# Kernel tuning notes

Hardware: AMD Instinct MI355X
Metric: run time of the kernel (lower is better)

## Reference

```python
import jax, jax.numpy as jnp
import numpy as np

N_FEAT = 128      # node_feat_size
HID = 128         # hidden_size
NUM_SEM = 64
N_ITER = 2
E_TYPES = 8
MAX_CHILDS = 65536
NUM_EDGES = 1048576


def setup_inputs() -> dict:
    key = jax.random.key(0)
    ks = jax.random.split(key, 12)
    d_in = N_FEAT + NUM_SEM
    inp = {
        "child_feats": jax.random.normal(ks[0], (1, MAX_CHILDS, d_in), jnp.float32),
        "child_exists": jax.random.uniform(ks[1], (1, MAX_CHILDS, 1), jnp.float32),
        "edge_type_onehot": jax.random.uniform(ks[2], (1, NUM_EDGES, E_TYPES), jnp.float32),
        "edge_indices": jax.random.randint(ks[3], (1, NUM_EDGES, 2), 0, MAX_CHILDS, jnp.int32),
        # learned params (PyTorch Linear: y = x @ W.T + b; store transposed)
        "W_child": jax.random.normal(ks[4], (d_in, HID), jnp.float32) / np.sqrt(d_in),
        "b_child": jnp.zeros((HID,), jnp.float32),
        "W_edge": jax.random.normal(ks[5], (N_ITER, 2 * HID + E_TYPES, HID), jnp.float32) / np.sqrt(2 * HID + E_TYPES),
        "b_edge": jnp.zeros((N_ITER, HID), jnp.float32),
        "W_parent": jax.random.normal(ks[6], ((N_ITER + 1) * HID, N_FEAT), jnp.float32) / np.sqrt((N_ITER + 1) * HID),
        "b_parent": jnp.zeros((N_FEAT,), jnp.float32),
    }
    return inp


def reference(child_feats, child_exists, edge_type_onehot, edge_indices,
              W_child, b_child, W_edge, b_edge, W_parent, b_parent):
    # batch_size == 1 enforced by original module
    x = jax.nn.relu(child_feats[0] @ W_child + b_child) * child_exists[0]  # (N, H)
    src = edge_indices[0, :, 0]  # (E,)
    dst = edge_indices[0, :, 1]  # (E,)
    ef = edge_type_onehot[0]     # (E, T)

    # node_symmetric_type == 'max' readout
    parent_feats = [jnp.max(x, axis=0)]
    for i in range(N_ITER):
        # gather endpoints, concat with edge features, small MLP
        nef = jnp.concatenate([x[src], x[dst], ef], axis=1)          # (E, 2H+T)
        nef = jax.nn.relu(nef @ W_edge[i] + b_edge[i])               # (E, H)
        # edge_symmetric_type == 'sum' -> scatter_add to source nodes
        x = jax.ops.segment_sum(nef, src, num_segments=MAX_CHILDS)   # (N, H)
        parent_feats.append(jnp.max(x, axis=0))

    parent_feat = jnp.concatenate(parent_feats)[None, :]             # (1, (I+1)*H)
    return jax.nn.relu(parent_feat @ W_parent + b_parent)            # (1, node_feat)
```

## Files before the change

kernel.cpp:

```cpp
#include <hip/hip_runtime.h>
#include <hip/hip_bf16.h>

#define HID 128
#define DIN 192
#define NCH 65536
#define NE  1048576

typedef __bf16 bfrag __attribute__((ext_vector_type(8)));
typedef float  ffrag __attribute__((ext_vector_type(4)));

static __device__ __forceinline__ __bf16 f2bf(float x) { return (__bf16)x; }
static __device__ __forceinline__ unsigned pk2(float a, float b) {
    __bf16 b0 = f2bf(a), b1 = f2bf(b);
    return (unsigned)*(unsigned short*)&b0 | ((unsigned)*(unsigned short*)&b1 << 16);
}

struct Frags { bfrag a[5]; };

__global__ __launch_bounds__(256) void k_child(
    const float* __restrict__ cf, const float* __restrict__ exists,
    const float* __restrict__ Wc, const float* __restrict__ bc,
    __bf16* __restrict__ xA, unsigned int* __restrict__ pmax)
{
    __shared__ __bf16 Wl[6 * 8 * 64 * 8];
    __shared__ float  bl[HID];
    __shared__ unsigned int cm[HID];
    const int t = threadIdx.x;

    for (int idx = t; idx < DIN * HID; idx += 256) {
        int k = idx >> 7, h = idx & 127;
        int kt = k >> 5, kk = k & 31;
        int lane = ((kk >> 3) << 4) | (h & 15);
        Wl[((((kt * 8) + (h >> 4)) * 64 + lane) << 3) | (kk & 7)] = f2bf(Wc[idx]);
    }
    for (int idx = t; idx < HID; idx += 256) { bl[idx] = bc[idx]; cm[idx] = 0u; }
    __syncthreads();

    const int wave = t >> 6, lane = t & 63;
    const int m = lane & 15, quad = lane >> 4;

    const int tile = blockIdx.x * 4 + wave;
    const int r0 = tile << 4;
    const int row = r0 + m;

    ffrag acc[8];
    #pragma unroll
    for (int u = 0; u < 8; ++u)
        #pragma unroll
        for (int r = 0; r < 4; ++r) acc[u][r] = 0.f;

    const float* arow = cf + (size_t)row * DIN + quad * 8;
    #pragma unroll
    for (int kt = 0; kt < 6; ++kt) {
        float4 f0 = *(const float4*)(arow + kt * 32);
        float4 f1 = *(const float4*)(arow + kt * 32 + 4);
        bfrag a;
        a[0]=f2bf(f0.x); a[1]=f2bf(f0.y); a[2]=f2bf(f0.z); a[3]=f2bf(f0.w);
        a[4]=f2bf(f1.x); a[5]=f2bf(f1.y); a[6]=f2bf(f1.z); a[7]=f2bf(f1.w);
        #pragma unroll
        for (int u = 0; u < 8; ++u) {
            bfrag b = *(const bfrag*)(&Wl[(((kt * 8 + u) * 64 + lane) << 3)]);
            acc[u] = __builtin_amdgcn_mfma_f32_16x16x32_bf16(a, b, acc[u], 0, 0, 0);
        }
    }

    float mxu[8];
    #pragma unroll
    for (int u = 0; u < 8; ++u) mxu[u] = 0.f;

    #pragma unroll
    for (int r = 0; r < 4; ++r) {
        int er = r0 + quad * 4 + r;
        float exv = exists[er];
        __bf16* orow = xA + (size_t)er * HID;
        #pragma unroll
        for (int u = 0; u < 8; ++u) {
            int col = u * 16 + m;
            float v = fmaxf(acc[u][r] + bl[col], 0.f) * exv;
            orow[col] = f2bf(v);
            mxu[u] = fmaxf(mxu[u], v);
        }
    }
    #pragma unroll
    for (int u = 0; u < 8; ++u) {
        float v = mxu[u];
        v = fmaxf(v, __shfl_xor(v, 16));
        v = fmaxf(v, __shfl_xor(v, 32));
        if (quad == 0) atomicMax(&cm[u * 16 + m], __float_as_uint(v));
    }
    __syncthreads();
    if (t < HID) atomicMax(&pmax[t], cm[t]);
}

__global__ __launch_bounds__(256) void k_hist(
    const int* __restrict__ eidx, int* __restrict__ deg)
{
    int e = blockIdx.x * 256 + threadIdx.x;
    atomicAdd(&deg[eidx[2 * e]], 1);
}

__global__ __launch_bounds__(1024) void k_scan(
    const int* __restrict__ deg, int* __restrict__ off, int* __restrict__ cursor)
{
    __shared__ int sc[1024];
    const int t = threadIdx.x;
    const int base = t * 64;
    int s = 0;
    for (int i = 0; i < 64; ++i) s += deg[base + i];
    sc[t] = s;
    __syncthreads();
    for (int o = 1; o < 1024; o <<= 1) {
        int v = (t >= o) ? sc[t - o] : 0;
        __syncthreads();
        sc[t] += v;
        __syncthreads();
    }
    int run = sc[t] - s;
    for (int i = 0; i < 64; ++i) {
        int v = deg[base + i];
        off[base + i] = run;
        cursor[base + i] = run;
        run += v;
    }
    if (t == 1023) off[NCH] = run;
}

__global__ __launch_bounds__(256) void k_scatter(
    const int* __restrict__ eidx, int* __restrict__ cursor,
    const float* __restrict__ ef,
    int* __restrict__ dsts, __bf16* __restrict__ efs)
{
    int e = blockIdx.x * 256 + threadIdx.x;
    int s = eidx[2 * e], d = eidx[2 * e + 1];
    const float4* p = (const float4*)(ef + (size_t)e * 8);
    float4 f0 = p[0], f1 = p[1];
    int pos = atomicAdd(&cursor[s], 1);
    dsts[pos] = d;
    uint4 pk;
    pk.x = pk2(f0.x, f0.y); pk.y = pk2(f0.z, f0.w);
    pk.z = pk2(f1.x, f1.y); pk.w = pk2(f1.z, f1.w);
    *(uint4*)(efs + (size_t)pos * 8) = pk;
}

__global__ __launch_bounds__(256) void k_src(
    __bf16* __restrict__ xCur, const float* __restrict__ We,
    const float* __restrict__ be, __bf16* __restrict__ St2)
{
    __shared__ __bf16 Wl[4 * 8 * 64 * 8];
    __shared__ float  bl[HID];
    const int t = threadIdx.x;
    const int wave = t >> 6, lane = t & 63;
    const int m = lane & 15, quad = lane >> 4;
    const int tile = blockIdx.x * 4 + wave;
    const int r0 = tile << 4;
    const int row = r0 + m;

    for (int idx = t; idx < 128 * HID; idx += 256) {
        int k = idx >> 7, h = idx & 127;
        int kt = k >> 5, kk = k & 31;
        int ln = ((kk >> 3) << 4) | (h & 15);
        Wl[((((kt * 8) + (h >> 4)) * 64 + ln) << 3) | (kk & 7)] = f2bf(We[idx]);
    }
    for (int idx = t; idx < HID; idx += 256) bl[idx] = be[idx];
    __syncthreads();

    bfrag a[4];
    const __bf16* ar = xCur + (size_t)row * HID + quad * 8;
    #pragma unroll
    for (int kt = 0; kt < 4; ++kt) a[kt] = *(const bfrag*)(ar + kt * 32);

    ffrag acc[8];
    #pragma unroll
    for (int u = 0; u < 8; ++u)
        #pragma unroll
        for (int r = 0; r < 4; ++r) acc[u][r] = 0.f;

    #pragma unroll
    for (int kt = 0; kt < 4; ++kt)
        #pragma unroll
        for (int u = 0; u < 8; ++u) {
            bfrag b = *(const bfrag*)(&Wl[(((kt * 8 + u) * 64 + lane) << 3)]);
            acc[u] = __builtin_amdgcn_mfma_f32_16x16x32_bf16(a[kt], b, acc[u], 0, 0, 0);
        }
    #pragma unroll
    for (int r = 0; r < 4; ++r) {
        int node = r0 + quad * 4 + r;
        bfrag pk;
        #pragma unroll
        for (int u = 0; u < 8; ++u) pk[u] = f2bf(acc[u][r] + bl[u * 16 + m]);
        *(bfrag*)(St2 + ((size_t)node * 16 + m) * 8) = pk;
    }
    __syncthreads();

    for (int idx = t; idx < 128 * HID; idx += 256) {
        int k = idx >> 7, h = idx & 127;
        int kt = k >> 5, kk = k & 31;
        int ln = ((kk >> 3) << 4) | (h & 15);
        Wl[((((kt * 8) + (h >> 4)) * 64 + ln) << 3) | (kk & 7)] = f2bf(We[(size_t)(128 + k) * HID + h]);
    }
    __syncthreads();

    #pragma unroll
    for (int u = 0; u < 8; ++u)
        #pragma unroll
        for (int r = 0; r < 4; ++r) acc[u][r] = 0.f;

    #pragma unroll
    for (int kt = 0; kt < 4; ++kt)
        #pragma unroll
        for (int u = 0; u < 8; ++u) {
            bfrag b = *(const bfrag*)(&Wl[(((kt * 8 + u) * 64 + lane) << 3)]);
            acc[u] = __builtin_amdgcn_mfma_f32_16x16x32_bf16(a[kt], b, acc[u], 0, 0, 0);
        }
    #pragma unroll
    for (int r = 0; r < 4; ++r) {
        int node = r0 + quad * 4 + r;
        __bf16* orow = xCur + (size_t)node * HID;
        #pragma unroll
        for (int u = 0; u < 8; ++u) orow[u * 16 + m] = f2bf(acc[u][r]);
    }
}

__global__ __launch_bounds__(256) void k_edge2(
    const __bf16* __restrict__ xCur,
    const int*    __restrict__ offs,
    const int*    __restrict__ dsts,
    const __bf16* __restrict__ efs,
    const __bf16* __restrict__ St2,
    const float*  __restrict__ We,
    __bf16* __restrict__ xNext,
    unsigned int* __restrict__ pmax, int stage)
{
    __shared__ __bf16 Wl[8 * 16 * 8];
    __shared__ unsigned int cm[HID];
    const int t = threadIdx.x;

    if (t < HID) cm[t] = 0u;
    for (int idx = t; idx < 8 * HID; idx += 256) {
        int k2 = idx >> 7, h = idx & 127;
        Wl[((((h >> 4) * 16) + (h & 15)) << 3) + k2] = f2bf(We[(size_t)(256 + k2) * HID + h]);
    }
    __syncthreads();

    const int wave = t >> 6, lane = t & 63;
    const int m = lane & 15, quad = lane >> 4;
    const int gw = blockIdx.x * 4 + wave;
    const int n0 = gw * 4;
    const int lc16 = (lane & 15) << 3;

    bfrag Bev, Bod;
    #pragma unroll
    for (int j = 0; j < 8; ++j) {
        Bev[j] = (quad == (m >> 3)     && j == (m & 7)) ? (__bf16)1.f : (__bf16)0.f;
        Bod[j] = (quad == 2 + (m >> 3) && j == (m & 7)) ? (__bf16)1.f : (__bf16)0.f;
    }

    const int o0 = offs[n0],     o1 = offs[n0 + 1], o2 = offs[n0 + 2];
    const int o3 = offs[n0 + 3], o4 = offs[n0 + 4];

    auto selo = [&](int q) -> int {
        return (q <= 0) ? o0 : (q == 1) ? o1 : (q == 2) ? o2 : (q == 3) ? o3 : o4;
    };

    float mxu[8];
    #pragma unroll
    for (int u = 0; u < 8; ++u) mxu[u] = 0.f;

    if (o0 < o4) {
        const int dvA = dsts[min(o0 + lane, o4 - 1)];
        const int dvB = dsts[min(o0 + 64 + lane, o4 - 1)];

        auto LOADT = [&](int j) -> Frags {
            Frags f;
            int jl = j + m; jl = (jl < o4) ? jl : (o4 - 1);
            int rel = jl - o0;
            int dA = __shfl(dvA, rel & 63);
            int dB = __shfl(dvB, rel & 63);
            int dm;
            if (rel < 64)       dm = dA;
            else if (rel < 128) dm = dB;
            else                dm = dsts[jl];
            const __bf16* rd = xCur + (size_t)dm * HID + quad * 8;
            f.a[0] = *(const bfrag*)(rd);
            f.a[1] = *(const bfrag*)(rd + 32);
            f.a[2] = *(const bfrag*)(rd + 64);
            f.a[3] = *(const bfrag*)(rd + 96);
            bfrag z;
            #pragma unroll
            for (int q = 0; q < 8; ++q) z[q] = (__bf16)0.f;
            if (quad == 0) z = *(const bfrag*)(efs + (size_t)jl * 8);
            f.a[4] = z;
            return f;
        };

        int ci = 0;
        while (selo(ci) == selo(ci + 1)) ++ci;
        int cj = selo(ci);

        bfrag sb = *(const bfrag*)(St2 + ((size_t)(n0 + ci) * 16 + m) * 8);
        float part[8];
        #pragma unroll
        for (int u = 0; u < 8; ++u) part[u] = 0.f;

        Frags aC = LOADT(cj);

        for (;;) {
            const int cEnd = selo(ci + 1);
            int ni = ci, nj = cj + 16;
            if (nj >= cEnd) {
                ni = ci + 1;
                while (ni < 4 && selo(ni) == selo(ni + 1)) ++ni;
                nj = (ni < 4) ? selo(ni) : 0;
            }
            const bool hn = (ni < 4);
            Frags aN;
            if (hn) aN = LOADT(nj);

            ffrag acc[8];
            #pragma unroll
            for (int u = 0; u < 8; ++u) {
                float s = (float)sb[u];
                acc[u][0] = s; acc[u][1] = s; acc[u][2] = s; acc[u][3] = s;
            }
            #pragma unroll
            for (int u = 0; u < 8; ++u)
                acc[u] = __builtin_amdgcn_mfma_f32_16x16x32_bf16(
                    aC.a[u >> 1], (u & 1) ? Bod : Bev, acc[u], 0, 0, 0);
            #pragma unroll
            for (int u = 0; u < 8; ++u) {
                bfrag b = *(const bfrag*)(&Wl[(u << 7) + lc16]);
                acc[u] = __builtin_amdgcn_mfma_f32_16x16x32_bf16(aC.a[4], b, acc[u], 0, 0, 0);
            }

            const int rb = cj + quad * 4;
            #pragma unroll
            for (int r = 0; r < 4; ++r) {
                if (rb + r < cEnd) {
                    #pragma unroll
                    for (int u = 0; u < 8; ++u)
                        part[u] += fmaxf(acc[u][r], 0.f);
                }
            }

            if (!hn || ni != ci) {
                float tot[8];
                #pragma unroll
                for (int u = 0; u < 8; ++u) {
                    float v = part[u];
                    v += __shfl_xor(v, 16);
                    v += __shfl_xor(v, 32);
                    tot[u] = v;
                    mxu[u] = fmaxf(mxu[u], v);
                }
                float sA = (quad == 0) ? tot[0] : (quad == 1) ? tot[2] : (quad == 2) ? tot[4] : tot[6];
                float sB = (quad == 0) ? tot[1] : (quad == 1) ? tot[3] : (quad == 2) ? tot[5] : tot[7];
                const int n = n0 + ci, u0 = quad * 2;
                xNext[(size_t)n * HID + u0 * 16 + m]      = f2bf(sA);
                xNext[(size_t)n * HID + u0 * 16 + 16 + m] = f2bf(sB);
                if (hn) {
                    sb = *(const bfrag*)(St2 + ((size_t)(n0 + ni) * 16 + m) * 8);
                    #pragma unroll
                    for (int u = 0; u < 8; ++u) part[u] = 0.f;
                }
            }
            if (!hn) break;
            aC = aN; ci = ni; cj = nj;
        }
    }

    {
        const int u0 = quad * 2;
        const __bf16 zz = (__bf16)0.f;
        if (o0 == o1) { xNext[(size_t)(n0+0)*HID + u0*16 + m] = zz; xNext[(size_t)(n0+0)*HID + u0*16 + 16 + m] = zz; }
        if (o1 == o2) { xNext[(size_t)(n0+1)*HID + u0*16 + m] = zz; xNext[(size_t)(n0+1)*HID + u0*16 + 16 + m] = zz; }
        if (o2 == o3) { xNext[(size_t)(n0+2)*HID + u0*16 + m] = zz; xNext[(size_t)(n0+2)*HID + u0*16 + 16 + m] = zz; }
        if (o3 == o4) { xNext[(size_t)(n0+3)*HID + u0*16 + m] = zz; xNext[(size_t)(n0+3)*HID + u0*16 + 16 + m] = zz; }
    }

    #pragma unroll
    for (int u = 0; u < 8; ++u) {
        float v = mxu[u];
        v = fmaxf(v, __shfl_xor(v, 16));
        v = fmaxf(v, __shfl_xor(v, 32));
        if (quad == 0) atomicMax(&cm[u * 16 + m], __float_as_uint(v));
    }
    __syncthreads();
    if (t < HID) atomicMax(&pmax[stage * HID + t], cm[t]);
}

__global__ __launch_bounds__(256) void k_edge_at(
    const __bf16* __restrict__ xA, const int* __restrict__ eidx,
    const float* __restrict__ ef, const float* __restrict__ We,
    const float* __restrict__ be, float* __restrict__ xNew)
{
    __shared__ __bf16 Wl[9 * 8 * 64 * 8];
    __shared__ float  bl[HID];
    const int t = threadIdx.x;
    for (int idx = t; idx < 8 * 64 * 8; idx += 256) Wl[8 * 8 * 64 * 8 + idx] = (__bf16)0.f;
    __syncthreads();
    for (int idx = t; idx < 256 * HID; idx += 256) {
        int k = idx >> 7, h = idx & 127;
        int kt = k >> 5, kk = k & 31;
        int lane = ((kk >> 3) << 4) | (h & 15);
        Wl[((((kt * 8) + (h >> 4)) * 64 + lane) << 3) | (kk & 7)] = f2bf(We[idx]);
    }
    for (int idx = t; idx < 8 * HID; idx += 256) {
        int k2 = idx >> 7, h = idx & 127;
        Wl[((((8 * 8) + (h >> 4)) * 64 + (h & 15)) << 3) | k2] = f2bf(We[(256 + k2) * HID + h]);
    }
    for (int idx = t; idx < HID; idx += 256) bl[idx] = be[idx];
    __syncthreads();

    const int wave = t >> 6, lane = t & 63;
    const int m = lane & 15, quad = lane >> 4;
    for (int c = 0; c < 8; ++c) {
        const int e0 = blockIdx.x * 512 + c * 64 + wave * 16;
        const int e  = e0 + m;
        const int src = eidx[2 * e], dst = eidx[2 * e + 1];
        const __bf16* rs = xA + (size_t)src * HID;
        const __bf16* rd = xA + (size_t)dst * HID;
        bfrag a[9];
        #pragma unroll
        for (int kt = 0; kt < 4; ++kt) a[kt] = *(const bfrag*)(rs + kt * 32 + quad * 8);
        #pragma unroll
        for (int kt = 4; kt < 8; ++kt) a[kt] = *(const bfrag*)(rd + (kt - 4) * 32 + quad * 8);
        {
            bfrag z;
            #pragma unroll
            for (int q = 0; q < 8; ++q) z[q] = (__bf16)0.f;
            if (quad == 0) {
                const float4* p = (const float4*)(ef + (size_t)e * 8);
                float4 f0 = p[0], f1 = p[1];
                z[0]=f2bf(f0.x); z[1]=f2bf(f0.y); z[2]=f2bf(f0.z); z[3]=f2bf(f0.w);
                z[4]=f2bf(f1.x); z[5]=f2bf(f1.y); z[6]=f2bf(f1.z); z[7]=f2bf(f1.w);
            }
            a[8] = z;
        }
        ffrag acc[8];
        #pragma unroll
        for (int u = 0; u < 8; ++u)
            #pragma unroll
            for (int r = 0; r < 4; ++r) acc[u][r] = 0.f;
        #pragma unroll
        for (int kt = 0; kt < 9; ++kt)
            #pragma unroll
            for (int u = 0; u < 8; ++u) {
                bfrag b = *(const bfrag*)(&Wl[(((kt * 8 + u) * 64 + lane) << 3)]);
                acc[u] = __builtin_amdgcn_mfma_f32_16x16x32_bf16(a[kt], b, acc[u], 0, 0, 0);
            }
        #pragma unroll
        for (int r = 0; r < 4; ++r) {
            int er = e0 + quad * 4 + r;
            int sr = eidx[2 * er];
            float* outrow = xNew + (size_t)sr * HID;
            #pragma unroll
            for (int u = 0; u < 8; ++u) {
                int col = u * 16 + m;
                atomicAdd(outrow + col, fmaxf(acc[u][r] + bl[col], 0.f));
            }
        }
    }
}

__global__ __launch_bounds__(256) void k_fin(
    float* __restrict__ xNew, __bf16* __restrict__ xA,
    unsigned int* __restrict__ pmax, int stage, int flags)
{
    const int t = threadIdx.x;
    const size_t total  = (size_t)NCH * HID;
    const size_t stride = (size_t)gridDim.x * 256;
    float mx = 0.f;
    for (size_t i = (size_t)blockIdx.x * 256 + t; i < total; i += stride) {
        float v = xNew[i];
        mx = fmaxf(mx, v);
        if (flags & 1) xA[i] = f2bf(v);
        if (flags & 2) xNew[i] = 0.f;
    }
    __shared__ float red[256];
    red[t] = mx;
    __syncthreads();
    if (t < 128) {
        float v = fmaxf(red[t], red[t + 128]);
        atomicMax(&pmax[stage * HID + t], __float_as_uint(v));
    }
}

__global__ __launch_bounds__(128) void k_parent(
    const unsigned int* __restrict__ pmaxU,
    const float* __restrict__ Wp, const float* __restrict__ bp,
    float* __restrict__ out)
{
    __shared__ float pl[384];
    const int t = threadIdx.x;
    for (int i = t; i < 384; i += 128) pl[i] = __uint_as_float(pmaxU[i]);
    __syncthreads();
    float acc = bp[t];
    for (int j = 0; j < 384; ++j) acc += pl[j] * Wp[j * HID + t];
    out[t] = fmaxf(acc, 0.f);
}

extern "C" void kernel_launch(void* const* d_in, const int* in_sizes, int n_in,
                              void* d_out, int out_size, void* d_ws, size_t ws_size,
                              hipStream_t stream)
{
    const float* cf   = (const float*)d_in[0];
    const float* ex   = (const float*)d_in[1];
    const float* ef   = (const float*)d_in[2];
    const int*   eidx = (const int*)d_in[3];
    const float* Wc   = (const float*)d_in[4];
    const float* bc   = (const float*)d_in[5];
    const float* We   = (const float*)d_in[6];
    const float* be   = (const float*)d_in[7];
    const float* Wp   = (const float*)d_in[8];
    const float* bp   = (const float*)d_in[9];
    float* out = (float*)d_out;

    char* ws = (char*)d_ws;

    const size_t OFF_XA   = 0;
    const size_t OFF_XB   = OFF_XA   + (size_t)NCH * HID * 2;
    const size_t OFF_ST   = OFF_XB   + (size_t)NCH * HID * 2;
    const size_t OFF_EFS  = OFF_ST   + (size_t)NCH * HID * 2;
    const size_t OFF_DST  = OFF_EFS  + (size_t)NE * 8 * 2;
    const size_t OFF_OFFS = OFF_DST  + (size_t)NE * 4;
    const size_t OFF_DEG  = OFF_OFFS + 262400;
    const size_t OFF_CUR  = OFF_DEG  + 262144;
    const size_t OFF_PMAX = OFF_CUR  + 262144;
    const size_t NEED     = OFF_PMAX + 2048;

    if (ws_size >= NEED) {
        __bf16*       xA   = (__bf16*)(ws + OFF_XA);
        __bf16*       xB   = (__bf16*)(ws + OFF_XB);
        __bf16*       St2  = (__bf16*)(ws + OFF_ST);
        __bf16*       efs  = (__bf16*)(ws + OFF_EFS);
        int*          dsts = (int*)   (ws + OFF_DST);
        int*          offs = (int*)   (ws + OFF_OFFS);
        int*          deg  = (int*)   (ws + OFF_DEG);
        int*          cur  = (int*)   (ws + OFF_CUR);
        unsigned int* pmax = (unsigned int*)(ws + OFF_PMAX);

        hipMemsetAsync(pmax, 0, 384 * sizeof(unsigned int), stream);
        hipMemsetAsync(deg, 0, NCH * sizeof(int), stream);

        k_child  <<<1024, 256, 0, stream>>>(cf, ex, Wc, bc, xA, pmax);
        k_hist   <<<4096, 256, 0, stream>>>(eidx, deg);
        k_scan   <<<1,   1024, 0, stream>>>(deg, offs, cur);
        k_scatter<<<4096, 256, 0, stream>>>(eidx, cur, ef, dsts, efs);

        k_src    <<<1024, 256, 0, stream>>>(xA, We, be, St2);
        k_edge2  <<<4096, 256, 0, stream>>>(xA, offs, dsts, efs, St2, We, xB, pmax, 1);
        k_src    <<<1024, 256, 0, stream>>>(xB, We + 264 * HID, be + HID, St2);
        k_edge2  <<<4096, 256, 0, stream>>>(xB, offs, dsts, efs, St2, We + 264 * HID, xA, pmax, 2);
        k_parent <<<1,    128, 0, stream>>>(pmax, Wp, bp, out);
    } else {
        float*        xNew = (float*)ws;
        __bf16*       xA   = (__bf16*)(ws + (size_t)NCH * HID * 4);
        unsigned int* pmax = (unsigned int*)(ws + (size_t)NCH * HID * 6);

        hipMemsetAsync(pmax, 0, 384 * sizeof(unsigned int), stream);
        hipMemsetAsync(xNew, 0, (size_t)NCH * HID * 4, stream);

        k_child  <<<1024, 256, 0, stream>>>(cf, ex, Wc, bc, xA, pmax);
        k_edge_at<<<2048, 256, 0, stream>>>(xA, eidx, ef, We,             be,       xNew);
        k_fin    <<<512,  256, 0, stream>>>(xNew, xA, pmax, 1, 3);
        k_edge_at<<<2048, 256, 0, stream>>>(xA, eidx, ef, We + 264 * HID, be + HID, xNew);
        k_fin    <<<512,  256, 0, stream>>>(xNew, xA, pmax, 2, 0);
        k_parent <<<1,    128, 0, stream>>>(pmax, Wp, bp, out);
    }
}
```

Before: 611.4 us.

## Fuse degree histogram into child kernel and parallelize the offset scan

The degree histogram now runs as extra blocks of the child-projection kernel, so the histogram atomics overlap the child GEMM and one launch is saved. The single-block 1024-thread serial scan is replaced by a three-kernel multi-block scan: per-block sums, a scan of block sums, then per-block local scans. The aim is to remove the long single-block scan, which reads 64 elements per thread serially. In exchange there are two extra launches and a small workspace increase; the fallback path passes a null deg pointer but never launches the histogram blocks.

After: 570.9 us. 1.07x faster.

```diff
diff --git a/kernel.cpp b/kernel.cpp
--- a/kernel.cpp
+++ b/kernel.cpp
@@ -17,11 +17,20 @@
 
 struct Frags { bfrag a[5]; };
 
-__global__ __launch_bounds__(256) void k_child(
+__global__ __launch_bounds__(256) void k_childhist(
     const float* __restrict__ cf, const float* __restrict__ exists,
     const float* __restrict__ Wc, const float* __restrict__ bc,
-    __bf16* __restrict__ xA, unsigned int* __restrict__ pmax)
-{
+    __bf16* __restrict__ xA, unsigned int* __restrict__ pmax,
+    const int* __restrict__ eidx, int* __restrict__ deg)
+{
+    if (blockIdx.x >= 1024) {
+        const int base = (blockIdx.x - 1024) * 1024 + threadIdx.x;
+        #pragma unroll
+        for (int k = 0; k < 4; ++k)
+            atomicAdd(&deg[eidx[2 * (base + k * 256)]], 1);
+        return;
+    }
+
     __shared__ __bf16 Wl[6 * 8 * 64 * 8];
     __shared__ float  bl[HID];
     __shared__ unsigned int cm[HID];
@@ -92,37 +101,55 @@
     if (t < HID) atomicMax(&pmax[t], cm[t]);
 }
 
-__global__ __launch_bounds__(256) void k_hist(
-    const int* __restrict__ eidx, int* __restrict__ deg)
-{
-    int e = blockIdx.x * 256 + threadIdx.x;
-    atomicAdd(&deg[eidx[2 * e]], 1);
-}
-
-__global__ __launch_bounds__(1024) void k_scan(
-    const int* __restrict__ deg, int* __restrict__ off, int* __restrict__ cursor)
-{
-    __shared__ int sc[1024];
+__global__ __launch_bounds__(256) void k_scan1(
+    const int* __restrict__ deg, int* __restrict__ bsum)
+{
+    const int b = blockIdx.x, t = threadIdx.x;
+    int v = deg[b * 256 + t];
+    #pragma unroll
+    for (int o = 1; o < 64; o <<= 1) v += __shfl_xor(v, o);
+    __shared__ int ws[4];
+    if ((t & 63) == 0) ws[t >> 6] = v;
+    __syncthreads();
+    if (t == 0) bsum[b] = ws[0] + ws[1] + ws[2] + ws[3];
+}
+
+__global__ __launch_bounds__(256) void k_scan2(
+    const int* __restrict__ bsum, int* __restrict__ bbase)
+{
+    __shared__ int sc[256];
     const int t = threadIdx.x;
-    const int base = t * 64;
-    int s = 0;
-    for (int i = 0; i < 64; ++i) s += deg[base + i];
-    sc[t] = s;
-    __syncthreads();
-    for (int o = 1; o < 1024; o <<= 1) {
-        int v = (t >= o) ? sc[t - o] : 0;
+    int v = bsum[t];
+    sc[t] = v;
+    __syncthreads();
+    for (int o = 1; o < 256; o <<= 1) {
+        int u = (t >= o) ? sc[t - o] : 0;
         __syncthreads();
-        sc[t] += v;
+        sc[t] += u;
         __syncthreads();
     }
-    int run = sc[t] - s;
-    for (int i = 0; i < 64; ++i) {
-        int v = deg[base + i];
-        off[base + i] = run;
-        cursor[base + i] = run;
-        run += v;
-    }
-    if (t == 1023) off[NCH] = run;
+    bbase[t] = sc[t] - v;
+}
+
+__global__ __launch_bounds__(256) void k_scan3(
+    const int* __restrict__ deg, const int* __restrict__ bbase,
+    int* __restrict__ off, int* __restrict__ cursor)
+{
+    __shared__ int sc[256];
+    const int b = blockIdx.x, t = threadIdx.x;
+    int v = deg[b * 256 + t];
+    sc[t] = v;
+    __syncthreads();
+    for (int o = 1; o < 256; o <<= 1) {
+        int u = (t >= o) ? sc[t - o] : 0;
+        __syncthreads();
+        sc[t] += u;
+        __syncthreads();
+    }
+    int excl = bbase[b] + sc[t] - v;
+    off[b * 256 + t] = excl;
+    cursor[b * 256 + t] = excl;
+    if (b == 255 && t == 255) off[NCH] = excl + v;
 }
 
 __global__ __launch_bounds__(256) void k_scatter(
@@ -526,7 +553,9 @@
     const size_t OFF_DEG  = OFF_OFFS + 262400;
     const size_t OFF_CUR  = OFF_DEG  + 262144;
     const size_t OFF_PMAX = OFF_CUR  + 262144;
-    const size_t NEED     = OFF_PMAX + 2048;
+    const size_t OFF_BS   = OFF_PMAX + 2048;
+    const size_t OFF_BB   = OFF_BS   + 1024;
+    const size_t NEED     = OFF_BB   + 1024;
 
     if (ws_size >= NEED) {
         __bf16*       xA   = (__bf16*)(ws + OFF_XA);
@@ -538,13 +567,16 @@
         int*          deg  = (int*)   (ws + OFF_DEG);
         int*          cur  = (int*)   (ws + OFF_CUR);
         unsigned int* pmax = (unsigned int*)(ws + OFF_PMAX);
+        int*          bsum = (int*)   (ws + OFF_BS);
+        int*          bbas = (int*)   (ws + OFF_BB);
 
         hipMemsetAsync(pmax, 0, 384 * sizeof(unsigned int), stream);
         hipMemsetAsync(deg, 0, NCH * sizeof(int), stream);
 
-        k_child  <<<1024, 256, 0, stream>>>(cf, ex, Wc, bc, xA, pmax);
-        k_hist   <<<4096, 256, 0, stream>>>(eidx, deg);
-        k_scan   <<<1,   1024, 0, stream>>>(deg, offs, cur);
+        k_childhist<<<2048, 256, 0, stream>>>(cf, ex, Wc, bc, xA, pmax, eidx, deg);
+        k_scan1  <<<256,  256, 0, stream>>>(deg, bsum);
+        k_scan2  <<<1,    256, 0, stream>>>(bsum, bbas);
+        k_scan3  <<<256,  256, 0, stream>>>(deg, bbas, offs, cur);
         k_scatter<<<4096, 256, 0, stream>>>(eidx, cur, ef, dsts, efs);
 
         k_src    <<<1024, 256, 0, stream>>>(xA, We, be, St2);
@@ -560,7 +592,7 @@
         hipMemsetAsync(pmax, 0, 384 * sizeof(unsigned int), stream);
         hipMemsetAsync(xNew, 0, (size_t)NCH * HID * 4, stream);
 
-        k_child  <<<1024, 256, 0, stream>>>(cf, ex, Wc, bc, xA, pmax);
+        k_childhist<<<1024, 256, 0, stream>>>(cf, ex, Wc, bc, xA, pmax, eidx, (int*)nullptr);
         k_edge_at<<<2048, 256, 0, stream>>>(xA, eidx, ef, We,             be,       xNew);
         k_fin    <<<512,  256, 0, stream>>>(xNew, xA, pmax, 1, 3);
         k_edge_at<<<2048, 256, 0, stream>>>(xA, eidx, ef, We + 264 * HID, be + HID, xNew);
```
